# Optimization experiments

Measured on AMD Instinct MI355X. Metric: run time of the kernel, lower is better.

The kernel has to match this reference:

```python
import jax, jax.numpy as jnp
import numpy as np

N = 100000
E = 1600000
IN_C, HID, HEADS, OUT_C = 128, 64, 4, 2
NEG_SLOPE = 0.2


def setup_inputs() -> dict:
    key = jax.random.key(0)
    ks = jax.random.split(key, 10)
    def glorot(k, shape):
        fan = shape[0] + shape[-1]
        return jax.random.uniform(k, shape, jnp.float32, -1.0, 1.0) * np.sqrt(6.0 / fan)
    x = jax.random.normal(ks[0], (N, IN_C), jnp.float32)
    edge_index = jax.random.randint(ks[1], (2, E), 0, N, jnp.int64)
    return {
        "x": x,
        "edge_index": edge_index,
        "W1": glorot(ks[2], (IN_C, HID)),
        "b1": jnp.zeros((HID,), jnp.float32),
        "W2": glorot(ks[3], (HID, HEADS * HID)),
        "att_src": glorot(ks[4], (HEADS, HID)) ,
        "att_dst": glorot(ks[5], (HEADS, HID)),
        "b2": jnp.zeros((HEADS * HID,), jnp.float32),
        "W3": glorot(ks[6], (HEADS * HID, OUT_C)),
        "b3": jnp.zeros((OUT_C,), jnp.float32),
    }


def _add_self_loops(edge_index, n):
    loop = jnp.arange(n, dtype=edge_index.dtype)
    src = jnp.concatenate([edge_index[0], loop])
    dst = jnp.concatenate([edge_index[1], loop])
    return src, dst


def gcn_conv(x, W, b, src, dst, n):
    # x' = X W, then symmetric deg-normalized scatter-add (self-loops included)
    xw = x @ W
    deg = jax.ops.segment_sum(jnp.ones_like(dst, dtype=xw.dtype), dst, num_segments=n)
    dinv = jnp.where(deg > 0, jax.lax.rsqrt(deg), 0.0)
    norm = dinv[src] * dinv[dst]                      # [E2]
    out = jax.ops.segment_sum(xw[src] * norm[:, None], dst, num_segments=n)
    return out + b


def gat_conv(x, W, att_src, att_dst, b, src, dst, n, heads, ch):
    xw = (x @ W).reshape(n, heads, ch)                # [N, H, C]
    a_s = (xw * att_src).sum(-1)                      # [N, H]
    a_d = (xw * att_dst).sum(-1)
    e = jax.nn.leaky_relu(a_s[src] + a_d[dst], NEG_SLOPE)   # [E2, H]
    # segment softmax over incoming edges per destination node
    m = jax.ops.segment_max(e, dst, num_segments=n)
    m = jnp.where(jnp.isfinite(m), m, 0.0)
    e = jnp.exp(e - m[dst])
    den = jax.ops.segment_sum(e, dst, num_segments=n)
    alpha = e / (den[dst] + 1e-16)                    # [E2, H]
    out = jax.ops.segment_sum(xw[src] * alpha[:, :, None], dst, num_segments=n)
    return out.reshape(n, heads * ch) + b


def reference(x, edge_index, W1, b1, W2, att_src, att_dst, b2, W3, b3):
    n = x.shape[0]
    src, dst = _add_self_loops(edge_index, n)
    h = jax.nn.relu(gcn_conv(x, W1, b1, src, dst, n))
    h = jax.nn.elu(gat_conv(h, W2, att_src, att_dst, b2, src, dst, n, HEADS, HID))
    return gcn_conv(h, W3, b3, src, dst, n)
```

## Files before the change

### kernel.cpp

```cpp
#include <hip/hip_runtime.h>
#include <math.h>

#define N_NODES 100000
#define N_EDGES 1600000
#define E2      (N_NODES + N_EDGES)
#define IN_C    128
#define HID     64
#define HEADS   4
#define HH      256
#define OUT_C   2
#define NEG_SLOPE 0.2f

#define SB   1024
#define NSB  ((N_NODES + SB - 1) / SB)
#define NRANGE 4
#define RDIV   25000
#define BINS   RDIV
#define BINW   (BINS / 2)
#define NBK    100
#define CHUNK  (N_EDGES / NBK)
#define C4     (CHUNK / 4)
#define CITER4 ((C4 + 255) / 256)
#define NHB    (NRANGE * NBK)
#define NFC    (N_EDGES / 256)
#define RT     10
#define NT1    6250
#define NGEMM1 ((NT1 + 3) / 4)

typedef __attribute__((ext_vector_type(8))) short bf16x8;
typedef __attribute__((ext_vector_type(4))) float f32x4;

__device__ __forceinline__ float bf2f(unsigned short u) {
    return __uint_as_float(((unsigned)u) << 16);
}
__device__ __forceinline__ unsigned short f2bf(float f) {
    unsigned u = __float_as_uint(f);
    u += 0x7fffu + ((u >> 16) & 1u);
    return (unsigned short)(u >> 16);
}


__global__ __launch_bounds__(256) void k_prep(const float* __restrict__ W2,
        const float* __restrict__ W1,
        const float* __restrict__ att_src, const float* __restrict__ att_dst,
        unsigned short* __restrict__ W2t, unsigned short* __restrict__ wsdt,
        unsigned short* __restrict__ W1t) {
    int b = blockIdx.x, t = threadIdx.x;
    if (b < 64) {
        int g = b * 256 + t;
        int k = g >> 8, n = g & 255;
        W2t[n * 64 + k] = f2bf(W2[g]);
        return;
    }
    if (b < 66) {
        int g = (b - 64) * 256 + t;
        wsdt[512 + g] = 0;
        int k = g >> 3, o = g & 7;
        int h = o & 3;
        const float* att = (o < 4) ? att_src : att_dst;
        float acc = 0.f;
        const float* wrow = W2 + (size_t)k * HH + h * 64;
        const float* arow = att + h * 64;
        for (int c = 0; c < 64; ++c) acc = fmaf(wrow[c], arow[c], acc);
        wsdt[o * 64 + k] = f2bf(acc);
        return;
    }
    int g = (b - 66) * 256 + t;
    int k = g >> 6, n = g & 63;
    W1t[n * 128 + k] = f2bf(W1[g]);
}

__global__ __launch_bounds__(256) void k_hist(const int* __restrict__ ei,
        unsigned short* __restrict__ hp16, unsigned short* __restrict__ rank16) {
    __shared__ unsigned int hh[BINW];
    int b = blockIdx.x, t = threadIdx.x;
    int r = b & 3, k = b >> 2;
    for (int i = t; i < BINW; i += 256) hh[i] = 0u;
    __syncthreads();
    const int4* dp4 = (const int4*)(ei + N_EDGES + (size_t)k * CHUNK);
    unsigned short* rp = rank16 + (size_t)k * CHUNK;
    int lo = r * RDIV;
#pragma unroll 2
    for (int it = 0; it < CITER4; ++it) {
        int i4 = it * 256 + t;
        if (i4 < C4) {
            int4 v = dp4[i4];
            int base = i4 * 4;
            int d0 = v.x - lo, d1 = v.y - lo, d2 = v.z - lo, d3 = v.w - lo;
            if ((unsigned)d0 < (unsigned)RDIV) {
                unsigned sh = (d0 & 1) * 16;
                unsigned old = atomicAdd(&hh[d0 >> 1], 1u << sh);
                rp[base + 0] = (unsigned short)(old >> sh);
            }
            if ((unsigned)d1 < (unsigned)RDIV) {
                unsigned sh = (d1 & 1) * 16;
                unsigned old = atomicAdd(&hh[d1 >> 1], 1u << sh);
                rp[base + 1] = (unsigned short)(old >> sh);
            }
            if ((unsigned)d2 < (unsigned)RDIV) {
                unsigned sh = (d2 & 1) * 16;
                unsigned old = atomicAdd(&hh[d2 >> 1], 1u << sh);
                rp[base + 2] = (unsigned short)(old >> sh);
            }
            if ((unsigned)d3 < (unsigned)RDIV) {
                unsigned sh = (d3 & 1) * 16;
                unsigned old = atomicAdd(&hh[d3 >> 1], 1u << sh);
                rp[base + 3] = (unsigned short)(old >> sh);
            }
        }
    }
    __syncthreads();
    unsigned* hp = (unsigned*)(hp16 + (size_t)(r * NBK + k) * BINS);
    for (int i = t; i < BINW; i += 256) hp[i] = hh[i];
}

__global__ __launch_bounds__(256) void k_scan1g(unsigned short* __restrict__ hp16,
        int* __restrict__ cnt, int* __restrict__ bsum,
        const float* __restrict__ x, const unsigned short* __restrict__ W1t,
        unsigned short* __restrict__ xw1b) {
    int b = blockIdx.x, t = threadIdx.x;
    if (b >= NSB) {
        int lane = t & 63, wv = t >> 6;
        int m = lane & 15, quad = lane >> 4;
        bf16x8 B[4][4];
#pragma unroll
        for (int ct = 0; ct < 4; ++ct)
#pragma unroll
            for (int ks = 0; ks < 4; ++ks)
                B[ct][ks] = *(const bf16x8*)(W1t + (size_t)(ct * 16 + m) * IN_C
                                             + ks * 32 + quad * 8);
        int tile = (b - NSB) * 4 + wv;
        if (tile >= NT1) return;
        int rbase = tile * 16;
        const float* xp = x + (size_t)(rbase + m) * IN_C + quad * 8;
        f32x4 c0 = {0.f, 0.f, 0.f, 0.f}, c1 = c0, c2 = c0, c3 = c0;
#pragma unroll
        for (int ks = 0; ks < 4; ++ks) {
            float4 f0 = *(const float4*)(xp + ks * 32);
            float4 f1 = *(const float4*)(xp + ks * 32 + 4);
            bf16x8 a;
            a[0] = (short)f2bf(f0.x); a[1] = (short)f2bf(f0.y);
            a[2] = (short)f2bf(f0.z); a[3] = (short)f2bf(f0.w);
            a[4] = (short)f2bf(f1.x); a[5] = (short)f2bf(f1.y);
            a[6] = (short)f2bf(f1.z); a[7] = (short)f2bf(f1.w);
            c0 = __builtin_amdgcn_mfma_f32_16x16x32_bf16(a, B[0][ks], c0, 0, 0, 0);
            c1 = __builtin_amdgcn_mfma_f32_16x16x32_bf16(a, B[1][ks], c1, 0, 0, 0);
            c2 = __builtin_amdgcn_mfma_f32_16x16x32_bf16(a, B[2][ks], c2, 0, 0, 0);
            c3 = __builtin_amdgcn_mfma_f32_16x16x32_bf16(a, B[3][ks], c3, 0, 0, 0);
        }
        int row0 = rbase + quad * 4;
#pragma unroll
        for (int ct = 0; ct < 4; ++ct) {
            f32x4 c = (ct == 0) ? c0 : (ct == 1) ? c1 : (ct == 2) ? c2 : c3;
            unsigned short* p = xw1b + (size_t)row0 * HID + ct * 16 + m;
#pragma unroll
            for (int r = 0; r < 4; ++r) p[(size_t)r * HID] = f2bf(c[r]);
        }
        return;
    }
    int s = 0;
#pragma unroll
    for (int u = 0; u < 4; ++u) {
        int i = b * SB + u * 256 + t;
        if (i < N_NODES) {
            int r = i / RDIV, bin = i - r * RDIV;
            unsigned short* p = hp16 + (size_t)r * NBK * BINS + bin;
            unsigned acc = 0;
            for (int k = 0; k < NBK; ++k) {
                unsigned short hv = p[(size_t)k * BINS];
                p[(size_t)k * BINS] = (unsigned short)acc;
                acc += hv;
            }
            cnt[i] = (int)acc;
            s += (int)acc + 1;
        }
    }
#pragma unroll
    for (int off = 1; off < 64; off <<= 1) s += __shfl_xor(s, off);
    __shared__ int wsum[4];
    int lane = t & 63, wv = t >> 6;
    if (lane == 0) wsum[wv] = s;
    __syncthreads();
    if (t == 0) bsum[b] = (wsum[0] + wsum[1]) + (wsum[2] + wsum[3]);
}

__global__ __launch_bounds__(256) void k_scan3(const int* __restrict__ cnt,
        const int* __restrict__ bsum, int* __restrict__ rowptr,
        float* __restrict__ dinv, int* __restrict__ col) {
    int b = blockIdx.x, t = threadIdx.x;
    int lane = t & 63, wv = t >> 6;
    __shared__ int wred[4];
    {
        int v = (t < b) ? bsum[t] : 0;
#pragma unroll
        for (int off = 1; off < 64; off <<= 1) v += __shfl_xor(v, off);
        if (lane == 0) wred[wv] = v;
    }
    __syncthreads();
    int pre = (wred[0] + wred[1]) + (wred[2] + wred[3]);
    __syncthreads();

    int i = b * SB + t * 4;
    int c0 = 0, c1 = 0, c2 = 0, c3 = 0;
    if (i + 3 < N_NODES) {
        int4 v = *(const int4*)(cnt + i);
        c0 = v.x; c1 = v.y; c2 = v.z; c3 = v.w;
    } else if (i < N_NODES) {
        c0 = cnt[i];
        if (i + 1 < N_NODES) c1 = cnt[i + 1];
        if (i + 2 < N_NODES) c2 = cnt[i + 2];
    }
    int n0 = (i < N_NODES), n1 = (i + 1 < N_NODES),
        n2 = (i + 2 < N_NODES), n3 = (i + 3 < N_NODES);
    int d0 = c0 + n0, d1 = c1 + n1, d2 = c2 + n2, d3 = c3 + n3;
    int s = (d0 + d1) + (d2 + d3);
    int inc = s;
#pragma unroll
    for (int off = 1; off < 64; off <<= 1) {
        int u = __shfl_up(inc, off);
        if (lane >= off) inc += u;
    }
    __shared__ int wtot[4];
    if (lane == 63) wtot[wv] = inc;
    __syncthreads();
    int base = pre + (inc - s);
    for (int w = 0; w < wv; ++w) base += wtot[w];
    if (n0) { rowptr[i]     = base;                dinv[i]     = rsqrtf((float)d0); col[base] = i; }
    if (n1) { rowptr[i + 1] = base + d0;           dinv[i + 1] = rsqrtf((float)d1); col[base + d0] = i + 1; }
    if (n2) { rowptr[i + 2] = base + d0 + d1;      dinv[i + 2] = rsqrtf((float)d2); col[base + d0 + d1] = i + 2; }
    if (n3) { rowptr[i + 3] = base + d0 + d1 + d2; dinv[i + 3] = rsqrtf((float)d3); col[base + d0 + d1 + d2] = i + 3; }
    if (b == 0 && t == 0) rowptr[N_NODES] = E2;
}

__global__ void k_fill(const int* __restrict__ ei, const int* __restrict__ rowptr,
        const unsigned short* __restrict__ hp16,
        const unsigned short* __restrict__ rank16, int* __restrict__ col) {
    int i = blockIdx.x * 256 + threadIdx.x;
    int d = ei[N_EDGES + i];
    int s = ei[i];
    int r = d / RDIV;
    int bin = d - r * RDIV;
    int k = i / CHUNK;
    unsigned pos = (unsigned)rowptr[d] + 1u
                 + (unsigned)hp16[(size_t)(r * NBK + k) * BINS + bin]
                 + (unsigned)rank16[i];
    col[pos] = s;
}

__global__ __launch_bounds__(256) void k_agg1(const int* __restrict__ rowptr,
        const int* __restrict__ col, const unsigned short* __restrict__ xw1b,
        const float* __restrict__ dinv, const float* __restrict__ b1,
        unsigned short* __restrict__ h1b) {
    int t = threadIdx.x;
    int lane = t & 63;
    int d = blockIdx.x * 4 + (t >> 6);
    if (d >= N_NODES) return;
    int start = rowptr[d], end = rowptr[d + 1];
    int sub = lane >> 4;
    int cpos = lane & 15;
    float4 acc = make_float4(0.f, 0.f, 0.f, 0.f);
    for (int base = start; base < end; base += 64) {
        int cnt = min(64, end - base);
        int sl = (base + lane < end) ? col[base + lane] : 0;
#pragma unroll 2
        for (int j = 0; j < cnt; j += 4) {
            int idx = j + sub;
            int sj = __shfl(sl, idx);
            if (idx < cnt) {
                float di = dinv[sj];
                ushort4 v = ((const ushort4*)(xw1b + (size_t)sj * HID))[cpos];
                acc.x = fmaf(di, bf2f(v.x), acc.x);
                acc.y = fmaf(di, bf2f(v.y), acc.y);
                acc.z = fmaf(di, bf2f(v.z), acc.z);
                acc.w = fmaf(di, bf2f(v.w), acc.w);
            }
        }
    }
    acc.x += __shfl_xor(acc.x, 16); acc.y += __shfl_xor(acc.y, 16);
    acc.z += __shfl_xor(acc.z, 16); acc.w += __shfl_xor(acc.w, 16);
    acc.x += __shfl_xor(acc.x, 32); acc.y += __shfl_xor(acc.y, 32);
    acc.z += __shfl_xor(acc.z, 32); acc.w += __shfl_xor(acc.w, 32);
    if (lane < 16) {
        float di = dinv[d];
        float4 b = ((const float4*)b1)[lane];
        float ox = fmaf(acc.x, di, b.x); ox = ox > 0.f ? ox : 0.f;
        float oy = fmaf(acc.y, di, b.y); oy = oy > 0.f ? oy : 0.f;
        float oz = fmaf(acc.z, di, b.z); oz = oz > 0.f ? oz : 0.f;
        float ow = fmaf(acc.w, di, b.w); ow = ow > 0.f ? ow : 0.f;
        ushort4 o = make_ushort4(f2bf(ox), f2bf(oy), f2bf(oz), f2bf(ow));
        ((ushort4*)(h1b + (size_t)d * HID))[lane] = o;
    }
}

__global__ __launch_bounds__(256) void k_attn(const unsigned short* __restrict__ h1b,
        const unsigned short* __restrict__ wsdt,
        float* __restrict__ a_s, float* __restrict__ a_d) {
    int t = threadIdx.x;
    int lane = t & 63, wv = t >> 6;
    int m = lane & 15, quad = lane >> 4;
    bf16x8 Bw0 = *(const bf16x8*)(wsdt + (size_t)m * 64 + quad * 8);
    bf16x8 Bw1 = *(const bf16x8*)(wsdt + (size_t)m * 64 + 32 + quad * 8);
    int tile = blockIdx.x * 4 + wv;
    if (tile >= NT1) return;
    int rbase = tile * 16;
    const unsigned short* ap = h1b + (size_t)(rbase + m) * 64 + quad * 8;
    bf16x8 a0 = *(const bf16x8*)(ap);
    bf16x8 a1 = *(const bf16x8*)(ap + 32);
    f32x4 aw = {0.f, 0.f, 0.f, 0.f};
    aw = __builtin_amdgcn_mfma_f32_16x16x32_bf16(a0, Bw0, aw, 0, 0, 0);
    aw = __builtin_amdgcn_mfma_f32_16x16x32_bf16(a1, Bw1, aw, 0, 0, 0);
    int row = rbase + quad * 4;
    if (m < 4) {
#pragma unroll
        for (int r = 0; r < 4; ++r) a_s[(row + r) * 4 + m] = aw[r];
    } else if (m < 8) {
#pragma unroll
        for (int r = 0; r < 4; ++r) a_d[(row + r) * 4 + (m - 4)] = aw[r];
    }
}

__global__ __launch_bounds__(256) void k_agg2u(const int* __restrict__ rowptr,
        const int* __restrict__ col, const unsigned short* __restrict__ h1b,
        const float* __restrict__ a_s, const float* __restrict__ a_d,
        unsigned short* __restrict__ ub, int dbase) {
    __shared__ int   ss[4][64];
    __shared__ float sp[4][64][4];
    int t = threadIdx.x;
    int lane = t & 63, wv = t >> 6;
    int sub = lane >> 4;
    int cpos = lane & 15;
    int d = dbase + blockIdx.x * 4 + wv;
    if (d >= N_NODES) return;
    const float4* as4 = (const float4*)a_s;
    float4 adv = ((const float4*)a_d)[d];
    int start = rowptr[d], end = rowptr[d + 1];

    float den0 = 0.f, den1 = 0.f, den2 = 0.f, den3 = 0.f;
    float4 A0 = make_float4(0.f, 0.f, 0.f, 0.f);
    float4 A1 = A0, A2 = A0, A3 = A0;
    for (int base = start; base < end; base += 64) {
        int cnt = min(64, end - base);
        float p0 = 0.f, p1 = 0.f, p2 = 0.f, p3 = 0.f;
        int s = 0;
        if (lane < cnt) {
            s = col[base + lane];
            float4 av = as4[s];
            float v;
            v = av.x + adv.x; v = v > 0.f ? v : NEG_SLOPE * v; p0 = __expf(v);
            v = av.y + adv.y; v = v > 0.f ? v : NEG_SLOPE * v; p1 = __expf(v);
            v = av.z + adv.z; v = v > 0.f ? v : NEG_SLOPE * v; p2 = __expf(v);
            v = av.w + adv.w; v = v > 0.f ? v : NEG_SLOPE * v; p3 = __expf(v);
            den0 += p0; den1 += p1; den2 += p2; den3 += p3;
        }
        ss[wv][lane] = s;
        ((float4*)sp[wv])[lane] = make_float4(p0, p1, p2, p3);
#pragma unroll 2
        for (int j = 0; j < cnt; j += 4) {
            int idx = j + sub;
            if (idx < cnt) {
                int sj = ss[wv][idx];
                float4 pj = ((const float4*)sp[wv])[idx];
                ushort4 v = ((const ushort4*)(h1b + (size_t)sj * 64u))[cpos];
                float c0 = bf2f(v.x), c1 = bf2f(v.y);
                float c2 = bf2f(v.z), c3 = bf2f(v.w);
                A0.x = fmaf(pj.x, c0, A0.x); A0.y = fmaf(pj.x, c1, A0.y);
                A0.z = fmaf(pj.x, c2, A0.z); A0.w = fmaf(pj.x, c3, A0.w);
                A1.x = fmaf(pj.y, c0, A1.x); A1.y = fmaf(pj.y, c1, A1.y);
                A1.z = fmaf(pj.y, c2, A1.z); A1.w = fmaf(pj.y, c3, A1.w);
                A2.x = fmaf(pj.z, c0, A2.x); A2.y = fmaf(pj.z, c1, A2.y);
                A2.z = fmaf(pj.z, c2, A2.z); A2.w = fmaf(pj.z, c3, A2.w);
                A3.x = fmaf(pj.w, c0, A3.x); A3.y = fmaf(pj.w, c1, A3.y);
                A3.z = fmaf(pj.w, c2, A3.z); A3.w = fmaf(pj.w, c3, A3.w);
            }
        }
    }
#pragma unroll
    for (int mk = 1; mk < 64; mk <<= 1) {
        den0 += __shfl_xor(den0, mk);
        den1 += __shfl_xor(den1, mk);
        den2 += __shfl_xor(den2, mk);
        den3 += __shfl_xor(den3, mk);
    }
#pragma unroll
    for (int mk = 16; mk < 64; mk <<= 1) {
        A0.x += __shfl_xor(A0.x, mk); A0.y += __shfl_xor(A0.y, mk);
        A0.z += __shfl_xor(A0.z, mk); A0.w += __shfl_xor(A0.w, mk);
        A1.x += __shfl_xor(A1.x, mk); A1.y += __shfl_xor(A1.y, mk);
        A1.z += __shfl_xor(A1.z, mk); A1.w += __shfl_xor(A1.w, mk);
        A2.x += __shfl_xor(A2.x, mk); A2.y += __shfl_xor(A2.y, mk);
        A2.z += __shfl_xor(A2.z, mk); A2.w += __shfl_xor(A2.w, mk);
        A3.x += __shfl_xor(A3.x, mk); A3.y += __shfl_xor(A3.y, mk);
        A3.z += __shfl_xor(A3.z, mk); A3.w += __shfl_xor(A3.w, mk);
    }
    if (lane < 16) {
        float r0 = 1.f / (den0 + 1e-16f), r1 = 1.f / (den1 + 1e-16f);
        float r2 = 1.f / (den2 + 1e-16f), r3 = 1.f / (den3 + 1e-16f);
        unsigned short* up = ub + (size_t)d * HH;
        ((ushort4*)(up))[cpos] = make_ushort4(
            f2bf(A0.x * r0), f2bf(A0.y * r0), f2bf(A0.z * r0), f2bf(A0.w * r0));
        ((ushort4*)(up + 64))[cpos] = make_ushort4(
            f2bf(A1.x * r1), f2bf(A1.y * r1), f2bf(A1.z * r1), f2bf(A1.w * r1));
        ((ushort4*)(up + 128))[cpos] = make_ushort4(
            f2bf(A2.x * r2), f2bf(A2.y * r2), f2bf(A2.z * r2), f2bf(A2.w * r2));
        ((ushort4*)(up + 192))[cpos] = make_ushort4(
            f2bf(A3.x * r3), f2bf(A3.y * r3), f2bf(A3.z * r3), f2bf(A3.w * r3));
    }
}

__global__ __launch_bounds__(256) void k_gemm3m(const unsigned short* __restrict__ ub,
        const unsigned short* __restrict__ W2t, const float* __restrict__ b2,
        const float* __restrict__ W3, const float* __restrict__ dinv,
        float2* __restrict__ xw3) {
    int t = threadIdx.x;
    int lane = t & 63, wv = t >> 6;
    int m = lane & 15, quad = lane >> 4;
    int nb = wv * 64 + m;
    bf16x8 B[4][2];
#pragma unroll
    for (int ct = 0; ct < 4; ++ct)
#pragma unroll
        for (int ks = 0; ks < 2; ++ks)
            B[ct][ks] = *(const bf16x8*)(W2t + (size_t)(nb + ct * 16) * 64
                                         + ks * 32 + quad * 8);
    float bv[4]; float2 w3v[4];
#pragma unroll
    for (int ct = 0; ct < 4; ++ct) {
        int n = nb + ct * 16;
        bv[ct] = b2[n];
        w3v[ct] = ((const float2*)W3)[n];
    }
    __shared__ float red[4][16][2];
    int r0 = blockIdx.x * (RT * 16);
    for (int tile = 0; tile < RT; ++tile) {
        int rbase = r0 + tile * 16;
        const unsigned short* ap = ub + (size_t)(rbase + m) * HH + wv * 64 + quad * 8;
        bf16x8 a0 = *(const bf16x8*)(ap);
        bf16x8 a1 = *(const bf16x8*)(ap + 32);
        f32x4 c0 = {0.f, 0.f, 0.f, 0.f}, c1 = c0, c2 = c0, c3 = c0;
        c0 = __builtin_amdgcn_mfma_f32_16x16x32_bf16(a0, B[0][0], c0, 0, 0, 0);
        c1 = __builtin_amdgcn_mfma_f32_16x16x32_bf16(a0, B[1][0], c1, 0, 0, 0);
        c2 = __builtin_amdgcn_mfma_f32_16x16x32_bf16(a0, B[2][0], c2, 0, 0, 0);
        c3 = __builtin_amdgcn_mfma_f32_16x16x32_bf16(a0, B[3][0], c3, 0, 0, 0);
        c0 = __builtin_amdgcn_mfma_f32_16x16x32_bf16(a1, B[0][1], c0, 0, 0, 0);
        c1 = __builtin_amdgcn_mfma_f32_16x16x32_bf16(a1, B[1][1], c1, 0, 0, 0);
        c2 = __builtin_amdgcn_mfma_f32_16x16x32_bf16(a1, B[2][1], c2, 0, 0, 0);
        c3 = __builtin_amdgcn_mfma_f32_16x16x32_bf16(a1, B[3][1], c3, 0, 0, 0);
        float px[4] = {0.f, 0.f, 0.f, 0.f}, py[4] = {0.f, 0.f, 0.f, 0.f};
#pragma unroll
        for (int ct = 0; ct < 4; ++ct) {
            f32x4 c = (ct == 0) ? c0 : (ct == 1) ? c1 : (ct == 2) ? c2 : c3;
#pragma unroll
            for (int r = 0; r < 4; ++r) {
                float o = c[r] + bv[ct];
                o = o > 0.f ? o : expm1f(o);
                px[r] = fmaf(o, w3v[ct].x, px[r]);
                py[r] = fmaf(o, w3v[ct].y, py[r]);
            }
        }
#pragma unroll
        for (int mk = 1; mk < 16; mk <<= 1) {
#pragma unroll
            for (int r = 0; r < 4; ++r) {
                px[r] += __shfl_xor(px[r], mk);
                py[r] += __shfl_xor(py[r], mk);
            }
        }
        if (m == 0) {
#pragma unroll
            for (int r = 0; r < 4; ++r) {
                red[wv][quad * 4 + r][0] = px[r];
                red[wv][quad * 4 + r][1] = py[r];
            }
        }
        __syncthreads();
        if (t < 32) {
            int row = t >> 1, xy = t & 1;
            float s = red[0][row][xy] + red[1][row][xy]
                    + red[2][row][xy] + red[3][row][xy];
            ((float*)(xw3 + (rbase + row)))[xy] = s * dinv[rbase + row];
        }
        __syncthreads();
    }
}

__global__ __launch_bounds__(256) void k_agg3(const int* __restrict__ rowptr,
        const int* __restrict__ col, const float2* __restrict__ xw3,
        const float* __restrict__ dinv, const float* __restrict__ b3,
        float* __restrict__ out) {
    int t = threadIdx.x;
    int lane = t & 63;
    int g = lane >> 2, s = lane & 3;
    int d = blockIdx.x * 64 + (t >> 6) * 16 + g;
    if (d >= N_NODES) return;
    int e0 = rowptr[d], e1 = rowptr[d + 1];
    float a0 = 0.f, a1 = 0.f;
    for (int e = e0 + s; e < e1; e += 4) {
        float2 v = xw3[col[e]];
        a0 += v.x; a1 += v.y;
    }
    a0 += __shfl_xor(a0, 1); a1 += __shfl_xor(a1, 1);
    a0 += __shfl_xor(a0, 2); a1 += __shfl_xor(a1, 2);
    if (s == 0) {
        float di = dinv[d];
        out[d * 2 + 0] = fmaf(a0, di, b3[0]);
        out[d * 2 + 1] = fmaf(a1, di, b3[1]);
    }
}


extern "C" void kernel_launch(void* const* d_in, const int* in_sizes, int n_in,
                              void* d_out, int out_size, void* d_ws, size_t ws_size,
                              hipStream_t stream) {
    const float* x       = (const float*)d_in[0];
    const int*   ei      = (const int*)d_in[1];
    const float* W1      = (const float*)d_in[2];
    const float* b1      = (const float*)d_in[3];
    const float* W2      = (const float*)d_in[4];
    const float* att_src = (const float*)d_in[5];
    const float* att_dst = (const float*)d_in[6];
    const float* b2      = (const float*)d_in[7];
    const float* W3      = (const float*)d_in[8];
    const float* b3      = (const float*)d_in[9];
    float* out = (float*)d_out;
    (void)in_sizes; (void)n_in; (void)out_size; (void)ws_size;

    char* ws = (char*)d_ws;
    size_t off = 0;
    auto alloc = [&](size_t bytes) -> void* {
        void* p = ws + off;
        off = (off + bytes + 255) & ~(size_t)255;
        return p;
    };
    int*    rowptr = (int*)alloc((N_NODES + 1) * sizeof(int));
    int*    cnt    = (int*)alloc(N_NODES * sizeof(int));
    int*    bsum   = (int*)alloc(NSB * sizeof(int));
    int*    col    = (int*)alloc((size_t)E2 * sizeof(int));
    float*  dinv   = (float*)alloc(N_NODES * sizeof(float));
    unsigned short* W2t  = (unsigned short*)alloc(64 * 256 * sizeof(unsigned short));
    unsigned short* wsdt = (unsigned short*)alloc(16 * 64 * sizeof(unsigned short));
    unsigned short* W1t  = (unsigned short*)alloc(64 * 128 * sizeof(unsigned short));
    unsigned short* xw1b = (unsigned short*)alloc((size_t)N_NODES * HID * sizeof(unsigned short));
    unsigned short* h1b  = (unsigned short*)alloc((size_t)N_NODES * HID * sizeof(unsigned short));
    float*  a_s    = (float*)alloc((size_t)N_NODES * HEADS * sizeof(float));
    float*  a_d    = (float*)alloc((size_t)N_NODES * HEADS * sizeof(float));
    unsigned short* ub   = (unsigned short*)alloc((size_t)N_NODES * HH * sizeof(unsigned short));
    float2* xw3    = (float2*)alloc((size_t)N_NODES * sizeof(float2));
    unsigned short* hp16   = ub;
    unsigned short* rank16 = ub + (size_t)NHB * BINS;

    k_prep<<<98, 256, 0, stream>>>(W2, W1, att_src, att_dst, W2t, wsdt, W1t);
    k_hist<<<NHB, 256, 0, stream>>>(ei, hp16, rank16);
    k_scan1g<<<NSB + NGEMM1, 256, 0, stream>>>(hp16, cnt, bsum, x, W1t, xw1b);
    k_scan3<<<NSB, 256, 0, stream>>>(cnt, bsum, rowptr, dinv, col);
    k_fill<<<NFC, 256, 0, stream>>>(ei, rowptr, hp16, rank16, col);

    k_agg1<<<(N_NODES + 3) / 4, 256, 0, stream>>>(rowptr, col, xw1b, dinv, b1, h1b);
    k_attn<<<(NT1 + 3) / 4, 256, 0, stream>>>(h1b, wsdt, a_s, a_d);
    const int HALF = 50000;
    k_agg2u<<<HALF / 4, 256, 0, stream>>>(rowptr, col, h1b, a_s, a_d, ub, 0);
    k_agg2u<<<(N_NODES - HALF + 3) / 4, 256, 0, stream>>>(rowptr, col, h1b, a_s, a_d, ub, HALF);
    k_gemm3m<<<(N_NODES / 16) / RT, 256, 0, stream>>>(ub, W2t, b2, W3, dinv, xw3);
    k_agg3<<<(N_NODES + 63) / 64, 256, 0, stream>>>(rowptr, col, xw3, dinv, b3, out);
}
```

Before: 387.4 us.

## Fuse attention-score projection into GCN aggregation and split layer-1 GEMM out

```diff
diff --git a/kernel.cpp b/kernel.cpp
--- a/kernel.cpp
+++ b/kernel.cpp
@@ -68,6 +68,47 @@
     int g = (b - 66) * 256 + t;
     int k = g >> 6, n = g & 63;
     W1t[n * 128 + k] = f2bf(W1[g]);
+}
+
+__global__ __launch_bounds__(256) void k_gemm1(const float* __restrict__ x,
+        const unsigned short* __restrict__ W1t, unsigned short* __restrict__ xw1b) {
+    int t = threadIdx.x;
+    int lane = t & 63, wv = t >> 6;
+    int m = lane & 15, quad = lane >> 4;
+    bf16x8 B[4][4];
+#pragma unroll
+    for (int ct = 0; ct < 4; ++ct)
+#pragma unroll
+        for (int ks = 0; ks < 4; ++ks)
+            B[ct][ks] = *(const bf16x8*)(W1t + (size_t)(ct * 16 + m) * IN_C
+                                         + ks * 32 + quad * 8);
+    int tile = blockIdx.x * 4 + wv;
+    if (tile >= NT1) return;
+    int rbase = tile * 16;
+    const float* xp = x + (size_t)(rbase + m) * IN_C + quad * 8;
+    f32x4 c0 = {0.f, 0.f, 0.f, 0.f}, c1 = c0, c2 = c0, c3 = c0;
+#pragma unroll
+    for (int ks = 0; ks < 4; ++ks) {
+        float4 f0 = *(const float4*)(xp + ks * 32);
+        float4 f1 = *(const float4*)(xp + ks * 32 + 4);
+        bf16x8 a;
+        a[0] = (short)f2bf(f0.x); a[1] = (short)f2bf(f0.y);
+        a[2] = (short)f2bf(f0.z); a[3] = (short)f2bf(f0.w);
+        a[4] = (short)f2bf(f1.x); a[5] = (short)f2bf(f1.y);
+        a[6] = (short)f2bf(f1.z); a[7] = (short)f2bf(f1.w);
+        c0 = __builtin_amdgcn_mfma_f32_16x16x32_bf16(a, B[0][ks], c0, 0, 0, 0);
+        c1 = __builtin_amdgcn_mfma_f32_16x16x32_bf16(a, B[1][ks], c1, 0, 0, 0);
+        c2 = __builtin_amdgcn_mfma_f32_16x16x32_bf16(a, B[2][ks], c2, 0, 0, 0);
+        c3 = __builtin_amdgcn_mfma_f32_16x16x32_bf16(a, B[3][ks], c3, 0, 0, 0);
+    }
+    int row0 = rbase + quad * 4;
+#pragma unroll
+    for (int ct = 0; ct < 4; ++ct) {
+        f32x4 c = (ct == 0) ? c0 : (ct == 1) ? c1 : (ct == 2) ? c2 : c3;
+        unsigned short* p = xw1b + (size_t)row0 * HID + ct * 16 + m;
+#pragma unroll
+        for (int r = 0; r < 4; ++r) p[(size_t)r * HID] = f2bf(c[r]);
+    }
 }
 
 __global__ __launch_bounds__(256) void k_hist(const int* __restrict__ ei,
@@ -114,50 +155,9 @@
     for (int i = t; i < BINW; i += 256) hp[i] = hh[i];
 }
 
-__global__ __launch_bounds__(256) void k_scan1g(unsigned short* __restrict__ hp16,
-        int* __restrict__ cnt, int* __restrict__ bsum,
-        const float* __restrict__ x, const unsigned short* __restrict__ W1t,
-        unsigned short* __restrict__ xw1b) {
+__global__ __launch_bounds__(256) void k_scan1(unsigned short* __restrict__ hp16,
+        int* __restrict__ cnt, int* __restrict__ bsum) {
     int b = blockIdx.x, t = threadIdx.x;
-    if (b >= NSB) {
-        int lane = t & 63, wv = t >> 6;
-        int m = lane & 15, quad = lane >> 4;
-        bf16x8 B[4][4];
-#pragma unroll
-        for (int ct = 0; ct < 4; ++ct)
-#pragma unroll
-            for (int ks = 0; ks < 4; ++ks)
-                B[ct][ks] = *(const bf16x8*)(W1t + (size_t)(ct * 16 + m) * IN_C
-                                             + ks * 32 + quad * 8);
-        int tile = (b - NSB) * 4 + wv;
-        if (tile >= NT1) return;
-        int rbase = tile * 16;
-        const float* xp = x + (size_t)(rbase + m) * IN_C + quad * 8;
-        f32x4 c0 = {0.f, 0.f, 0.f, 0.f}, c1 = c0, c2 = c0, c3 = c0;
-#pragma unroll
-        for (int ks = 0; ks < 4; ++ks) {
-            float4 f0 = *(const float4*)(xp + ks * 32);
-            float4 f1 = *(const float4*)(xp + ks * 32 + 4);
-            bf16x8 a;
-            a[0] = (short)f2bf(f0.x); a[1] = (short)f2bf(f0.y);
-            a[2] = (short)f2bf(f0.z); a[3] = (short)f2bf(f0.w);
-            a[4] = (short)f2bf(f1.x); a[5] = (short)f2bf(f1.y);
-            a[6] = (short)f2bf(f1.z); a[7] = (short)f2bf(f1.w);
-            c0 = __builtin_amdgcn_mfma_f32_16x16x32_bf16(a, B[0][ks], c0, 0, 0, 0);
-            c1 = __builtin_amdgcn_mfma_f32_16x16x32_bf16(a, B[1][ks], c1, 0, 0, 0);
-            c2 = __builtin_amdgcn_mfma_f32_16x16x32_bf16(a, B[2][ks], c2, 0, 0, 0);
-            c3 = __builtin_amdgcn_mfma_f32_16x16x32_bf16(a, B[3][ks], c3, 0, 0, 0);
-        }
-        int row0 = rbase + quad * 4;
-#pragma unroll
-        for (int ct = 0; ct < 4; ++ct) {
-            f32x4 c = (ct == 0) ? c0 : (ct == 1) ? c1 : (ct == 2) ? c2 : c3;
-            unsigned short* p = xw1b + (size_t)row0 * HID + ct * 16 + m;
-#pragma unroll
-            for (int r = 0; r < 4; ++r) p[(size_t)r * HID] = f2bf(c[r]);
-        }
-        return;
-    }
     int s = 0;
 #pragma unroll
     for (int u = 0; u < 4; ++u) {
@@ -247,10 +247,12 @@
     col[pos] = s;
 }
 
-__global__ __launch_bounds__(256) void k_agg1(const int* __restrict__ rowptr,
+__global__ __launch_bounds__(256) void k_agg1a(const int* __restrict__ rowptr,
         const int* __restrict__ col, const unsigned short* __restrict__ xw1b,
         const float* __restrict__ dinv, const float* __restrict__ b1,
-        unsigned short* __restrict__ h1b) {
+        const unsigned short* __restrict__ wsdt,
+        unsigned short* __restrict__ h1b,
+        float* __restrict__ a_s, float* __restrict__ a_d) {
     int t = threadIdx.x;
     int lane = t & 63;
     int d = blockIdx.x * 4 + (t >> 6);
@@ -261,13 +263,14 @@
     float4 acc = make_float4(0.f, 0.f, 0.f, 0.f);
     for (int base = start; base < end; base += 64) {
         int cnt = min(64, end - base);
-        int sl = (base + lane < end) ? col[base + lane] : 0;
+        int sl = 0; float dl = 0.f;
+        if (base + lane < end) { sl = col[base + lane]; dl = dinv[sl]; }
 #pragma unroll 2
         for (int j = 0; j < cnt; j += 4) {
             int idx = j + sub;
             int sj = __shfl(sl, idx);
+            float di = __shfl(dl, idx);
             if (idx < cnt) {
-                float di = dinv[sj];
                 ushort4 v = ((const ushort4*)(xw1b + (size_t)sj * HID))[cpos];
                 acc.x = fmaf(di, bf2f(v.x), acc.x);
                 acc.y = fmaf(di, bf2f(v.y), acc.y);
@@ -280,42 +283,31 @@
     acc.z += __shfl_xor(acc.z, 16); acc.w += __shfl_xor(acc.w, 16);
     acc.x += __shfl_xor(acc.x, 32); acc.y += __shfl_xor(acc.y, 32);
     acc.z += __shfl_xor(acc.z, 32); acc.w += __shfl_xor(acc.w, 32);
-    if (lane < 16) {
-        float di = dinv[d];
-        float4 b = ((const float4*)b1)[lane];
-        float ox = fmaf(acc.x, di, b.x); ox = ox > 0.f ? ox : 0.f;
-        float oy = fmaf(acc.y, di, b.y); oy = oy > 0.f ? oy : 0.f;
-        float oz = fmaf(acc.z, di, b.z); oz = oz > 0.f ? oz : 0.f;
-        float ow = fmaf(acc.w, di, b.w); ow = ow > 0.f ? ow : 0.f;
-        ushort4 o = make_ushort4(f2bf(ox), f2bf(oy), f2bf(oz), f2bf(ow));
-        ((ushort4*)(h1b + (size_t)d * HID))[lane] = o;
-    }
-}
-
-__global__ __launch_bounds__(256) void k_attn(const unsigned short* __restrict__ h1b,
-        const unsigned short* __restrict__ wsdt,
-        float* __restrict__ a_s, float* __restrict__ a_d) {
-    int t = threadIdx.x;
-    int lane = t & 63, wv = t >> 6;
-    int m = lane & 15, quad = lane >> 4;
-    bf16x8 Bw0 = *(const bf16x8*)(wsdt + (size_t)m * 64 + quad * 8);
-    bf16x8 Bw1 = *(const bf16x8*)(wsdt + (size_t)m * 64 + 32 + quad * 8);
-    int tile = blockIdx.x * 4 + wv;
-    if (tile >= NT1) return;
-    int rbase = tile * 16;
-    const unsigned short* ap = h1b + (size_t)(rbase + m) * 64 + quad * 8;
-    bf16x8 a0 = *(const bf16x8*)(ap);
-    bf16x8 a1 = *(const bf16x8*)(ap + 32);
-    f32x4 aw = {0.f, 0.f, 0.f, 0.f};
-    aw = __builtin_amdgcn_mfma_f32_16x16x32_bf16(a0, Bw0, aw, 0, 0, 0);
-    aw = __builtin_amdgcn_mfma_f32_16x16x32_bf16(a1, Bw1, aw, 0, 0, 0);
-    int row = rbase + quad * 4;
-    if (m < 4) {
-#pragma unroll
-        for (int r = 0; r < 4; ++r) a_s[(row + r) * 4 + m] = aw[r];
-    } else if (m < 8) {
-#pragma unroll
-        for (int r = 0; r < 4; ++r) a_d[(row + r) * 4 + (m - 4)] = aw[r];
+    float di = dinv[d];
+    float4 b = ((const float4*)b1)[cpos];
+    float h0 = fmaf(acc.x, di, b.x); h0 = h0 > 0.f ? h0 : 0.f;
+    float h1 = fmaf(acc.y, di, b.y); h1 = h1 > 0.f ? h1 : 0.f;
+    float h2 = fmaf(acc.z, di, b.z); h2 = h2 > 0.f ? h2 : 0.f;
+    float h3 = fmaf(acc.w, di, b.w); h3 = h3 > 0.f ? h3 : 0.f;
+    ushort4 o = make_ushort4(f2bf(h0), f2bf(h1), f2bf(h2), f2bf(h3));
+    if (lane < 16)
+        ((ushort4*)(h1b + (size_t)d * HID))[cpos] = o;
+    float r0 = bf2f(o.x), r1 = bf2f(o.y), r2 = bf2f(o.z), r3 = bf2f(o.w);
+    int hsel = lane >> 4;
+    const unsigned short* ws = wsdt + hsel * 64 + cpos * 4;
+    const unsigned short* wd = wsdt + (hsel + 4) * 64 + cpos * 4;
+    float ps = r0 * bf2f(ws[0]) + r1 * bf2f(ws[1])
+             + r2 * bf2f(ws[2]) + r3 * bf2f(ws[3]);
+    float pd = r0 * bf2f(wd[0]) + r1 * bf2f(wd[1])
+             + r2 * bf2f(wd[2]) + r3 * bf2f(wd[3]);
+#pragma unroll
+    for (int mk = 1; mk < 16; mk <<= 1) {
+        ps += __shfl_xor(ps, mk);
+        pd += __shfl_xor(pd, mk);
+    }
+    if (cpos == 0) {
+        a_s[d * 4 + hsel] = ps;
+        a_d[d * 4 + hsel] = pd;
     }
 }
 
@@ -549,13 +541,14 @@
     unsigned short* rank16 = ub + (size_t)NHB * BINS;
 
     k_prep<<<98, 256, 0, stream>>>(W2, W1, att_src, att_dst, W2t, wsdt, W1t);
+    k_gemm1<<<NGEMM1, 256, 0, stream>>>(x, W1t, xw1b);
     k_hist<<<NHB, 256, 0, stream>>>(ei, hp16, rank16);
-    k_scan1g<<<NSB + NGEMM1, 256, 0, stream>>>(hp16, cnt, bsum, x, W1t, xw1b);
+    k_scan1<<<NSB, 256, 0, stream>>>(hp16, cnt, bsum);
     k_scan3<<<NSB, 256, 0, stream>>>(cnt, bsum, rowptr, dinv, col);
     k_fill<<<NFC, 256, 0, stream>>>(ei, rowptr, hp16, rank16, col);
 
-    k_agg1<<<(N_NODES + 3) / 4, 256, 0, stream>>>(rowptr, col, xw1b, dinv, b1, h1b);
-    k_attn<<<(NT1 + 3) / 4, 256, 0, stream>>>(h1b, wsdt, a_s, a_d);
+    k_agg1a<<<(N_NODES + 3) / 4, 256, 0, stream>>>(rowptr, col, xw1b, dinv, b1,
+                                                   wsdt, h1b, a_s, a_d);
     const int HALF = 50000;
     k_agg2u<<<HALF / 4, 256, 0, stream>>>(rowptr, col, h1b, a_s, a_d, ub, 0);
     k_agg2u<<<(N_NODES - HALF + 3) / 4, 256, 0, stream>>>(rowptr, col, h1b, a_s, a_d, ub, HALF);
```

After: 393.9 us. About the same (+1.7%).
